# Performance work log

Hardware: AMD Instinct MI355X
Metric: run time of the kernel (lower is better)

The kernel has to match this reference:

```python
import jax, jax.numpy as jnp
import numpy as np

B, L, D, H, F = 2, 1024, 1024, 16, 4096
DH = D // H
EPS = 1e-6


def _layernorm(x, g, b, eps=1e-5):
    m = jnp.mean(x, axis=-1, keepdims=True)
    v = jnp.mean((x - m) ** 2, axis=-1, keepdims=True)
    return (x - m) / jnp.sqrt(v + eps) * g + b


def setup_inputs() -> dict:
    key = jax.random.key(0)
    ks = jax.random.split(key, 12)

    def w(k, shape):
        return jax.random.normal(k, shape, dtype=jnp.float32) * 0.02

    return {
        "inputs": jax.random.normal(ks[0], (B, L, D), dtype=jnp.float32),
        "attn_mask": jnp.zeros((L, L), dtype=jnp.bool_),
        "Wq": w(ks[1], (D, D)), "bq": jnp.zeros((D,), jnp.float32),
        "Wk": w(ks[2], (D, D)), "bk": jnp.zeros((D,), jnp.float32),
        "Wv": w(ks[3], (D, D)), "bv": jnp.zeros((D,), jnp.float32),
        "Wo": w(ks[4], (D, D)), "bo": jnp.zeros((D,), jnp.float32),
        "ln1_g": jnp.ones((D,), jnp.float32), "ln1_b": jnp.zeros((D,), jnp.float32),
        "W1": w(ks[5], (D, F)), "b1": jnp.zeros((F,), jnp.float32),
        "W2": w(ks[6], (F, D)), "b2": jnp.zeros((D,), jnp.float32),
        "ln2_g": jnp.ones((D,), jnp.float32), "ln2_b": jnp.zeros((D,), jnp.float32),
    }


def _decoder_layer(inputs, Wq, bq, Wk, bk, Wv, bv, Wo, bo,
                   ln1_g, ln1_b, W1, b1, W2, b2, ln2_g, ln2_b):
    Bn, Ln, Dn = inputs.shape

    def heads(W, b):
        # [B,L,D] -> [B,H,L,Dh]
        return (inputs @ W + b).reshape(Bn, Ln, H, DH).transpose(0, 2, 1, 3)

    q = jax.nn.sigmoid(heads(Wq, bq))  # kernel feature map
    k = jax.nn.sigmoid(heads(Wk, bk))
    v = heads(Wv, bv)

    normal = (jnp.arange(Ln, dtype=jnp.float32) + 1.0)[None, None, :]  # [1,1,L]

    sink_in = normal / jnp.einsum('bhld,bhld->bhl', q + EPS, jnp.cumsum(k, axis=2) + EPS)
    src_out = normal / jnp.einsum('bhld,bhld->bhl', k + EPS, jnp.cumsum(q, axis=2) + EPS)

    cons_sink = jnp.einsum('bhld,bhld->bhl', q + EPS,
                           jnp.cumsum(k * src_out[..., None], axis=2) + EPS) / normal
    cons_src = jnp.einsum('bhld,bhld->bhl', k + EPS,
                          jnp.cumsum(q * sink_in[..., None], axis=2) + EPS) / normal
    cons_src = jnp.clip(cons_src, -1.0, 1.0)

    sink_alloc = jax.nn.sigmoid(cons_sink)
    cons_src = jnp.exp(cons_src)
    src_comp = cons_src / jnp.cumsum(cons_src, axis=-1) * normal

    # causal linear attention: cumsum of outer products k v^T, contracted with q
    qs = q * (sink_in / normal)[..., None]           # [B,H,L,Dh]
    vs = v * src_comp[..., None]                     # [B,H,L,Dh]
    kv = jnp.cumsum(jnp.einsum('bhld,bhlm->bhldm', k, vs), axis=2)  # [B,H,L,Dh,Dh]
    x = jnp.einsum('bhld,bhldm->bhlm', qs, kv) * sink_alloc[..., None]

    x = x.transpose(0, 2, 1, 3).reshape(Bn, Ln, Dn)
    attn = x @ Wo + bo

    h = _layernorm(inputs + attn, ln1_g, ln1_b)
    ffn = jax.nn.gelu(h @ W1 + b1, approximate=False) @ W2 + b2
    return _layernorm(h + ffn, ln2_g, ln2_b)


def reference(inputs, attn_mask, Wq, bq, Wk, bk, Wv, bv, Wo, bo,
              ln1_g, ln1_b, W1, b1, W2, b2, ln2_g, ln2_b):
    # attn_mask is unused by the original module (causality comes from cumsum)
    return _decoder_layer(inputs, Wq, bq, Wk, bk, Wv, bv, Wo, bo,
                          ln1_g, ln1_b, W1, b1, W2, b2, ln2_g, ln2_b)
```

## Files before the change

### kernel.cpp

```cpp
#include <hip/hip_runtime.h>
#include <hip/hip_bf16.h>

#define EPS 1e-6f
#define NBH 32
#define LSEQ 1024
#define DHD 64

typedef unsigned short u16;
typedef __bf16 bf16x8 __attribute__((ext_vector_type(8)));
typedef float f32x4 __attribute__((ext_vector_type(4)));

__device__ inline u16 f2bf(float f){
  union { float f; unsigned u; } un; un.f = f;
  unsigned u = un.u;
  u += 0x7fffu + ((u >> 16) & 1u);
  return (u16)(u >> 16);
}

__device__ inline float wred64(float v){
#pragma unroll
  for (int off = 32; off > 0; off >>= 1) v += __shfl_xor(v, off, 64);
  return v;
}

__device__ inline float wscan64(float v, int lane){
  float run = v;
#pragma unroll
  for (int off = 1; off < 64; off <<= 1){
    float t = __shfl_up(run, off, 64);
    if (lane >= off) run += t;
  }
  return run;
}

__device__ inline float fast_sigmoid(float x){
  return 1.f / (1.f + __expf(-x));
}

__device__ inline void gload_lds16(const u16* g, u16* l){
  __builtin_amdgcn_global_load_lds(
      (const __attribute__((address_space(1))) unsigned int*)g,
      (__attribute__((address_space(3))) unsigned int*)l, 16, 0, 0);
}

__global__ __launch_bounds__(256) void f2bf_kernel(const float* __restrict__ in,
                                                   u16* __restrict__ out, int n4){
  int i = blockIdx.x * 256 + threadIdx.x;
  if (i < n4){
    float4 v = reinterpret_cast<const float4*>(in)[i];
    ushort4 o; o.x = f2bf(v.x); o.y = f2bf(v.y); o.z = f2bf(v.z); o.w = f2bf(v.w);
    reinterpret_cast<ushort4*>(out)[i] = o;
  }
}

__device__ inline void tr_tile2(const float* in, u16* out, int R, int C, int r0, int c0){
  __shared__ float tile[32][33];
  int x = threadIdx.x & 31, y = threadIdx.x >> 5;
#pragma unroll
  for (int j = 0; j < 4; j++)
    tile[y + j*8][x] = in[(size_t)(r0 + y + j*8) * C + c0 + x];
  __syncthreads();
#pragma unroll
  for (int j = 0; j < 4; j++)
    out[(size_t)(c0 + y + j*8) * R + r0 + x] = f2bf(tile[x][y + j*8]);
}

__global__ __launch_bounds__(256) void transpose4_f2bf(
    const float* __restrict__ w0, const float* __restrict__ w1,
    const float* __restrict__ w2, const float* __restrict__ w3,
    u16* __restrict__ dqkv, u16* __restrict__ dwo){
  int z = blockIdx.z;
  const float* in = (z == 0) ? w0 : (z == 1) ? w1 : (z == 2) ? w2 : w3;
  u16* out = (z < 3) ? (dqkv + (size_t)z * 1024 * 1024) : dwo;
  tr_tile2(in, out, 1024, 1024, blockIdx.y * 32, blockIdx.x * 32);
}

__global__ __launch_bounds__(256) void transpose2_f2bf(
    const float* __restrict__ w1, const float* __restrict__ w2,
    u16* __restrict__ d1, u16* __restrict__ d2){
  if (blockIdx.z == 0)
    tr_tile2(w1, d1, 1024, 4096, blockIdx.y * 32, blockIdx.x * 32);
  else
    tr_tile2(w2, d2, 4096, 1024, blockIdx.x * 32, blockIdx.y * 32);
}

__global__ __launch_bounds__(256) void bias_gather(const float* __restrict__ bq,
                                                   const float* __restrict__ bk,
                                                   const float* __restrict__ bv,
                                                   float* __restrict__ dst){
  int i = blockIdx.x * 256 + threadIdx.x;
  if (i < 3072){
    float v = (i < 1024) ? bq[i] : (i < 2048) ? bk[i - 1024] : bv[i - 2048];
    dst[i] = v;
  }
}

template<int BM, int BN, int ACT, int OM>
__global__ __launch_bounds__(256) void gemm_mfma(
    const u16* __restrict__ A, const u16* __restrict__ Bt,
    const float* __restrict__ bias, const float* __restrict__ resid,
    float* __restrict__ outF, u16* __restrict__ outB,
    int M, int N, int K)
{
  constexpr int BK = 64;
  constexpr int MI = BM / 32;
  constexpr int NJ = BN / 32;
  constexpr int RA = BM / 32;
  constexpr int RB = BN / 32;
  constexpr int NS = RA + RB;
  __shared__ u16 As[2][BM * BK];
  __shared__ u16 Bs[2][BN * BK];
  const int tid = threadIdx.x;
  const int lane = tid & 63, wave = tid >> 6;
  const int lrow = lane & 15, lg = lane >> 4;
  const int m0 = blockIdx.x * BM, n0 = blockIdx.y * BN;
  const int wm = (wave >> 1) * (BM / 2), wn = (wave & 1) * (BN / 2);

  const int ksz = K / gridDim.z;
  const int k_begin = blockIdx.z * ksz;
  const int k_end = k_begin + ksz;

  f32x4 acc[MI][NJ];
#pragma unroll
  for (int i = 0; i < MI; i++)
#pragma unroll
    for (int j = 0; j < NJ; j++) acc[i][j] = (f32x4){0.f, 0.f, 0.f, 0.f};

  const u16* Ab = A + (size_t)m0 * K;
  const u16* Bb = Bt + (size_t)n0 * K;

  const int s0 = ((0 * 4 + lg) ^ (lrow & 7)) * 8;
  const int s1 = ((1 * 4 + lg) ^ (lrow & 7)) * 8;

  auto STAGE = [&](int buf, int k0){
#pragma unroll
    for (int r = 0; r < RA; ++r){
      int c = r * 256 + tid;
      int row = c >> 3;
      int kk = ((c ^ row) & 7) << 3;
      gload_lds16(Ab + (size_t)row * K + k0 + kk, &As[buf][(r * 256 + wave * 64) * 8]);
    }
#pragma unroll
    for (int r = 0; r < RB; ++r){
      int c = r * 256 + tid;
      int row = c >> 3;
      int kk = ((c ^ row) & 7) << 3;
      gload_lds16(Bb + (size_t)row * K + k0 + kk, &Bs[buf][(r * 256 + wave * 64) * 8]);
    }
  };

  STAGE(0, k_begin);
  int cur = 0;
  for (int k0 = k_begin; k0 < k_end; k0 += BK){
    if (k0 + BK < k_end){
      STAGE(cur ^ 1, k0 + BK);
      if constexpr (NS == 8)      asm volatile("s_waitcnt vmcnt(8)" ::: "memory");
      else if constexpr (NS == 6) asm volatile("s_waitcnt vmcnt(6)" ::: "memory");
      else                        asm volatile("s_waitcnt vmcnt(0)" ::: "memory");
    } else {
      asm volatile("s_waitcnt vmcnt(0)" ::: "memory");
    }
    __builtin_amdgcn_s_barrier();
    __builtin_amdgcn_sched_barrier(0);
#pragma unroll
    for (int kh = 0; kh < 2; ++kh){
      const int ss = (kh == 0) ? s0 : s1;
      bf16x8 af[MI], bfv[NJ];
#pragma unroll
      for (int i = 0; i < MI; ++i)
        af[i] = *reinterpret_cast<const bf16x8*>(&As[cur][(wm + i * 16 + lrow) * BK + ss]);
#pragma unroll
      for (int j = 0; j < NJ; ++j)
        bfv[j] = *reinterpret_cast<const bf16x8*>(&Bs[cur][(wn + j * 16 + lrow) * BK + ss]);
#pragma unroll
      for (int i = 0; i < MI; ++i)
#pragma unroll
        for (int j = 0; j < NJ; ++j)
          acc[i][j] = __builtin_amdgcn_mfma_f32_16x16x32_bf16(af[i], bfv[j], acc[i][j], 0, 0, 0);
    }
    __builtin_amdgcn_s_barrier();
    cur ^= 1;
  }

#pragma unroll
  for (int i = 0; i < MI; ++i){
#pragma unroll
    for (int j = 0; j < NJ; ++j){
      int col = n0 + wn + j * 16 + lrow;
      float bv = (OM != 4 && bias) ? bias[col] : 0.f;
#pragma unroll
      for (int r = 0; r < 4; ++r){
        int row = m0 + wm + i * 16 + lg * 4 + r;
        float x = acc[i][j][r] + bv;
        if (OM == 1){
          if (col < 2048) x = fast_sigmoid(x);
          int which = col >> 10, cc = col & 1023, h = cc >> 6, d = cc & 63;
          int b = row >> 10, l = row & 1023;
          outF[(size_t)which * (2048ull * 1024) +
               (((size_t)(b * 16 + h)) * 1024 + l) * 64 + d] = x;
        } else if (OM == 4){
          outF[((size_t)blockIdx.z * M + row) * N + col] = x;
        } else {
          if (ACT == 2){
            float u = 0.7978845608f * (x + 0.044715f * x * x * x);
            float e = __expf(2.f * u);
            x = 0.5f * x * (2.f - 2.f / (e + 1.f));
          }
          outB[(size_t)row * N + col] = f2bf(x);
        }
      }
    }
  }
}

__global__ __launch_bounds__(256) void chunk_sums(const float* __restrict__ k, const float* __restrict__ q,
                                                  float* __restrict__ ck, float* __restrict__ cq){
  int blk = blockIdx.x;
  int lane = threadIdx.x & 63, wave = threadIdx.x >> 6;
  size_t base = (size_t)blk * 64 * DHD;
  float sk = 0.f, sq = 0.f;
  for (int l = wave * 16; l < wave * 16 + 16; l++){
    sk += k[base + l * 64 + lane];
    sq += q[base + l * 64 + lane];
  }
  __shared__ float rd[2][4][64];
  rd[0][wave][lane] = sk; rd[1][wave][lane] = sq;
  __syncthreads();
  if (wave == 0){
    ck[(size_t)blk * 64 + lane] = rd[0][0][lane] + rd[0][1][lane] + rd[0][2][lane] + rd[0][3][lane];
    cq[(size_t)blk * 64 + lane] = rd[1][0][lane] + rd[1][1][lane] + rd[1][2][lane] + rd[1][3][lane];
  }
}

__global__ __launch_bounds__(256) void sink_tile(
    const float* __restrict__ q, const float* __restrict__ k,
    const float* __restrict__ ck, const float* __restrict__ cq,
    float* __restrict__ sink_in, float* __restrict__ src_out,
    float* __restrict__ cso, float* __restrict__ cqsi)
{
  int blk = blockIdx.x, bh = blk >> 4, c = blk & 15;
  int tid = threadIdx.x, lane = tid & 63, wave = tid >> 6;
  __shared__ float qT[64][65], kT[64][65], G[64][66];
  __shared__ float PK[64], PQ[64];
  __shared__ float rk[64], rq[64], crk[64], crq[64], siv[64], sov[64];
  __shared__ float rd[2][4][64];
  size_t base = ((size_t)bh * LSEQ + c * 64) * DHD;
  const float* qb = q + base; const float* kb = k + base;
  for (int c4 = tid; c4 < 1024; c4 += 256){
    int l = c4 >> 4, d0 = (c4 & 15) * 4;
    float4 qv = *reinterpret_cast<const float4*>(qb + c4 * 4);
    qT[d0+0][l] = qv.x; qT[d0+1][l] = qv.y; qT[d0+2][l] = qv.z; qT[d0+3][l] = qv.w;
    float4 kv = *reinterpret_cast<const float4*>(kb + c4 * 4);
    kT[d0+0][l] = kv.x; kT[d0+1][l] = kv.y; kT[d0+2][l] = kv.z; kT[d0+3][l] = kv.w;
  }
  if (tid < 64){
    float pk = 0.f, pq = 0.f;
    for (int cc = 0; cc < c; cc++){
      pk += ck[((size_t)bh * 16 + cc) * 64 + tid];
      pq += cq[((size_t)bh * 16 + cc) * 64 + tid];
    }
    PK[tid] = pk; PQ[tid] = pq;
  }
  __syncthreads();
  float sumPK = wred64(PK[lane]);
  float sumPQ = wred64(PQ[lane]);
  {
    int l = lane, g = wave;
    float qrow[64];
#pragma unroll
    for (int d = 0; d < 64; d++) qrow[d] = qT[d][l];
    float p[16] = {};
    for (int d = 0; d < 64; d++){
      float qv = qrow[d];
#pragma unroll
      for (int j4 = 0; j4 < 4; j4++){
        float4 kk = *reinterpret_cast<const float4*>(&kT[d][g * 16 + j4 * 4]);
        p[j4*4+0] += qv * kk.x; p[j4*4+1] += qv * kk.y;
        p[j4*4+2] += qv * kk.z; p[j4*4+3] += qv * kk.w;
      }
    }
#pragma unroll
    for (int jj = 0; jj < 16; jj++) G[l][g * 16 + jj] = p[jj];
  }
  {
    float pk_ = 0.f, pq_ = 0.f;
#pragma unroll
    for (int d = wave * 16; d < wave * 16 + 16; d++){
      pk_ += kT[d][lane]; pq_ += qT[d][lane];
    }
    rd[0][wave][lane] = pk_; rd[1][wave][lane] = pq_;
  }
  __syncthreads();
  if (tid < 64){
    rk[tid] = rd[0][0][tid] + rd[0][1][tid] + rd[0][2][tid] + rd[0][3][tid];
    rq[tid] = rd[1][0][tid] + rd[1][1][tid] + rd[1][2][tid] + rd[1][3][tid];
  }
  __syncthreads();
  if (wave == 0)      crk[lane] = wscan64(rk[lane], lane);
  else if (wave == 1) crq[lane] = wscan64(rq[lane], lane);
  __syncthreads();
  {
    int l = lane;
    float p1 = 0.f, p2 = 0.f;
#pragma unroll
    for (int j = wave * 16; j < wave * 16 + 16; j++){
      float g1 = (j <= l) ? G[l][j] : 0.f;
      p1 += g1 + qT[j][l] * PK[j];
      float g2 = (j <= l) ? G[j][l] : 0.f;
      p2 += g2 + kT[j][l] * PQ[j];
    }
    rd[0][wave][l] = p1; rd[1][wave][l] = p2;
  }
  __syncthreads();
  const float EPS2 = 64.f * EPS * EPS;
  if (tid < 64){
    int l = tid;
    float s1 = rd[0][0][l] + rd[0][1][l] + rd[0][2][l] + rd[0][3][l];
    float s2 = rd[1][0][l] + rd[1][1][l] + rd[1][2][l] + rd[1][3][l];
    int L = c * 64 + l; float nrm = (float)(L + 1);
    float den1 = s1 + EPS * rq[l] + EPS * (sumPK + crk[l]) + EPS2;
    float den2 = s2 + EPS * rk[l] + EPS * (sumPQ + crq[l]) + EPS2;
    float si_ = nrm / den1, so_ = nrm / den2;
    sink_in[(size_t)bh * LSEQ + L] = si_;
    src_out[(size_t)bh * LSEQ + L] = so_;
    siv[l] = si_; sov[l] = so_;
  }
  __syncthreads();
  float s1 = 0.f, s2 = 0.f;
  for (int l = wave * 16; l < wave * 16 + 16; l++){
    s1 += sov[l] * kT[lane][l];
    s2 += siv[l] * qT[lane][l];
  }
  rd[0][wave][lane] = s1; rd[1][wave][lane] = s2;
  __syncthreads();
  if (wave == 0){
    cso [(size_t)blk * 64 + lane] = rd[0][0][lane] + rd[0][1][lane] + rd[0][2][lane] + rd[0][3][lane];
    cqsi[(size_t)blk * 64 + lane] = rd[1][0][lane] + rd[1][1][lane] + rd[1][2][lane] + rd[1][3][lane];
  }
}

__global__ __launch_bounds__(256) void cons_tile(
    const float* __restrict__ q, const float* __restrict__ k,
    const float* __restrict__ cso, const float* __restrict__ cqsi,
    const float* __restrict__ sink_in, const float* __restrict__ src_out,
    float* __restrict__ sa, float* __restrict__ ebuf)
{
  int blk = blockIdx.x, bh = blk >> 4, c = blk & 15;
  int tid = threadIdx.x, lane = tid & 63, wave = tid >> 6;
  __shared__ float qT[64][65], kT[64][65], G[64][66];
  __shared__ float PKso[64], PQsi[64];
  __shared__ float rk[64], rq[64], cwrk[64], cwrq[64], siv[64], sov[64];
  __shared__ float rd[2][4][64];
  size_t base = ((size_t)bh * LSEQ + c * 64) * DHD;
  const float* qb = q + base; const float* kb = k + base;
  for (int c4 = tid; c4 < 1024; c4 += 256){
    int l = c4 >> 4, d0 = (c4 & 15) * 4;
    float4 qv = *reinterpret_cast<const float4*>(qb + c4 * 4);
    qT[d0+0][l] = qv.x; qT[d0+1][l] = qv.y; qT[d0+2][l] = qv.z; qT[d0+3][l] = qv.w;
    float4 kv = *reinterpret_cast<const float4*>(kb + c4 * 4);
    kT[d0+0][l] = kv.x; kT[d0+1][l] = kv.y; kT[d0+2][l] = kv.z; kT[d0+3][l] = kv.w;
  }
  if (tid < 64){
    float pk = 0.f, pq = 0.f;
    for (int cc = 0; cc < c; cc++){
      pk += cso [((size_t)bh * 16 + cc) * 64 + tid];
      pq += cqsi[((size_t)bh * 16 + cc) * 64 + tid];
    }
    PKso[tid] = pk; PQsi[tid] = pq;
  } else if (tid < 128){
    int l = tid - 64;
    sov[l] = src_out[(size_t)bh * LSEQ + c * 64 + l];
    siv[l] = sink_in[(size_t)bh * LSEQ + c * 64 + l];
  }
  __syncthreads();
  float sumPKso = wred64(PKso[lane]);
  float sumPQsi = wred64(PQsi[lane]);
  {
    int l = lane, g = wave;
    float qrow[64];
#pragma unroll
    for (int d = 0; d < 64; d++) qrow[d] = qT[d][l];
    float p[16] = {};
    for (int d = 0; d < 64; d++){
      float qv = qrow[d];
#pragma unroll
      for (int j4 = 0; j4 < 4; j4++){
        float4 kk = *reinterpret_cast<const float4*>(&kT[d][g * 16 + j4 * 4]);
        p[j4*4+0] += qv * kk.x; p[j4*4+1] += qv * kk.y;
        p[j4*4+2] += qv * kk.z; p[j4*4+3] += qv * kk.w;
      }
    }
#pragma unroll
    for (int jj = 0; jj < 16; jj++) G[l][g * 16 + jj] = p[jj];
  }
  {
    float pk_ = 0.f, pq_ = 0.f;
#pragma unroll
    for (int d = wave * 16; d < wave * 16 + 16; d++){
      pk_ += kT[d][lane]; pq_ += qT[d][lane];
    }
    rd[0][wave][lane] = pk_; rd[1][wave][lane] = pq_;
  }
  __syncthreads();
  if (tid < 64){
    rk[tid] = rd[0][0][tid] + rd[0][1][tid] + rd[0][2][tid] + rd[0][3][tid];
    rq[tid] = rd[1][0][tid] + rd[1][1][tid] + rd[1][2][tid] + rd[1][3][tid];
  }
  __syncthreads();
  if (wave == 0)      cwrk[lane] = wscan64(sov[lane] * rk[lane], lane);
  else if (wave == 1) cwrq[lane] = wscan64(siv[lane] * rq[lane], lane);
  __syncthreads();
  {
    int l = lane;
    float p3 = 0.f, p4 = 0.f;
#pragma unroll
    for (int j = wave * 16; j < wave * 16 + 16; j++){
      float g3 = (j <= l) ? sov[j] * G[l][j] : 0.f;
      p3 += g3 + qT[j][l] * PKso[j];
      float g4 = (j <= l) ? siv[j] * G[j][l] : 0.f;
      p4 += g4 + kT[j][l] * PQsi[j];
    }
    rd[0][wave][l] = p3; rd[1][wave][l] = p4;
  }
  __syncthreads();
  const float EPS2 = 64.f * EPS * EPS;
  if (tid < 64){
    int l = tid;
    float s3 = rd[0][0][l] + rd[0][1][l] + rd[0][2][l] + rd[0][3][l];
    float s4 = rd[1][0][l] + rd[1][1][l] + rd[1][2][l] + rd[1][3][l];
    int L = c * 64 + l; float nrm = (float)(L + 1);
    float cs = (s3 + EPS * rq[l] + EPS * (sumPKso + cwrk[l]) + EPS2) / nrm;
    sa[(size_t)bh * LSEQ + L] = fast_sigmoid(cs);
    float c2 = (s4 + EPS * rk[l] + EPS * (sumPQsi + cwrq[l]) + EPS2) / nrm;
    c2 = fminf(1.f, fmaxf(-1.f, c2));
    ebuf[(size_t)bh * LSEQ + L] = __expf(c2);
  }
}

__global__ __launch_bounds__(64) void srccomp_kernel(const float* __restrict__ ebuf, float* __restrict__ sc){
  int bh = blockIdx.x; int lane = threadIdx.x;
  const float* eb = ebuf + (size_t)bh * LSEQ;
  float loc[16]; float s = 0.f;
#pragma unroll
  for (int i = 0; i < 16; i++){ loc[i] = eb[lane * 16 + i]; s += loc[i]; }
  float run = wscan64(s, lane);
  float acc = run - s;
  float* scb = sc + (size_t)bh * LSEQ;
#pragma unroll
  for (int i = 0; i < 16; i++){
    acc += loc[i];
    scb[lane * 16 + i] = loc[i] / acc * (float)(lane * 16 + i + 1);
  }
}

__global__ __launch_bounds__(256) void phaseA(const float* __restrict__ k, const float* __restrict__ v,
                                              const float* __restrict__ sc, float* __restrict__ S){
  int blk = blockIdx.x; int bh = blk >> 4, c = blk & 15;
  __shared__ float ks[64][68], vss[64][68];
  __shared__ float vc[64];
  int tid = threadIdx.x;
  size_t base = ((size_t)bh * LSEQ + c * 64) * DHD;
  const float* kb = k + base; const float* vb = v + base;
  if (tid < 64) vc[tid] = sc[(size_t)bh * LSEQ + c * 64 + tid];
  __syncthreads();
  for (int c4 = tid; c4 < 1024; c4 += 256){
    int l = c4 >> 4, d0 = (c4 & 15) * 4;
    *reinterpret_cast<float4*>(&ks[l][d0]) = *reinterpret_cast<const float4*>(kb + c4 * 4);
    float4 vv = *reinterpret_cast<const float4*>(vb + c4 * 4);
    float w = vc[l];
    vss[l][d0+0] = vv.x * w; vss[l][d0+1] = vv.y * w;
    vss[l][d0+2] = vv.z * w; vss[l][d0+3] = vv.w * w;
  }
  __syncthreads();
  int m = tid >> 2, dg = tid & 3;
  float acc[16] = {};
  for (int l = 0; l < 64; l++){
    float vm = vss[l][m];
#pragma unroll
    for (int d4 = 0; d4 < 4; d4++){
      float4 kk = *reinterpret_cast<const float4*>(&ks[l][dg * 16 + d4 * 4]);
      acc[d4*4+0] += vm * kk.x; acc[d4*4+1] += vm * kk.y;
      acc[d4*4+2] += vm * kk.z; acc[d4*4+3] += vm * kk.w;
    }
  }
  float* Sb = S + (size_t)blk * 4096 + m * 64 + dg * 16;
#pragma unroll
  for (int d4 = 0; d4 < 4; d4++)
    *reinterpret_cast<float4*>(Sb + d4 * 4) =
        make_float4(acc[d4*4], acc[d4*4+1], acc[d4*4+2], acc[d4*4+3]);
}

__global__ __launch_bounds__(256) void phaseB(const float* __restrict__ S, float* __restrict__ KVp){
  int blk = blockIdx.x; int bh = blk >> 4, c = blk & 15;
  int off = threadIdx.x * 16;
  float acc[16] = {};
  for (int cc = 0; cc < c; cc++){
    size_t idx = ((size_t)bh * 16 + cc) * 4096 + off;
#pragma unroll
    for (int t = 0; t < 4; t++){
      float4 sv = *reinterpret_cast<const float4*>(S + idx + t * 4);
      acc[t*4] += sv.x; acc[t*4+1] += sv.y; acc[t*4+2] += sv.z; acc[t*4+3] += sv.w;
    }
  }
  size_t oidx = ((size_t)bh * 16 + c) * 4096 + off;
#pragma unroll
  for (int t = 0; t < 4; t++)
    *reinterpret_cast<float4*>(KVp + oidx + t * 4) =
        make_float4(acc[t*4], acc[t*4+1], acc[t*4+2], acc[t*4+3]);
}

__global__ __launch_bounds__(256) void phaseC(const float* __restrict__ q, const float* __restrict__ k,
                                              const float* __restrict__ v, const float* __restrict__ KVp,
                                              const float* __restrict__ sink_in, const float* __restrict__ sc,
                                              const float* __restrict__ sa, u16* __restrict__ x){
  int blk = blockIdx.x; int bh = blk >> 4, c = blk & 15;
  int b = bh >> 4, h = bh & 15;
  __shared__ float qsT[64][65];
  __shared__ float kT[64][68];
  __shared__ float vss[64][68];
  __shared__ float kvs[64][68];
  __shared__ float Ps[64][66];
  __shared__ float qc[64], vc[64];
  int tid = threadIdx.x;
  size_t base = ((size_t)bh * LSEQ + c * 64) * DHD;
  const float* qb = q + base; const float* kb = k + base; const float* vb = v + base;
  const float* kvb = KVp + (size_t)blk * 4096;
  if (tid < 64){
    int L = c * 64 + tid;
    qc[tid] = sink_in[(size_t)bh * LSEQ + L] / (float)(L + 1);
    vc[tid] = sc[(size_t)bh * LSEQ + L];
  }
  __syncthreads();
  for (int c4 = tid; c4 < 1024; c4 += 256){
    int l = c4 >> 4, d0 = (c4 & 15) * 4;
    float qw = qc[l], vw = vc[l];
    float4 qv = *reinterpret_cast<const float4*>(qb + c4 * 4);
    qsT[d0+0][l] = qv.x * qw; qsT[d0+1][l] = qv.y * qw;
    qsT[d0+2][l] = qv.z * qw; qsT[d0+3][l] = qv.w * qw;
    float4 kv4 = *reinterpret_cast<const float4*>(kb + c4 * 4);
    kT[d0+0][l] = kv4.x; kT[d0+1][l] = kv4.y; kT[d0+2][l] = kv4.z; kT[d0+3][l] = kv4.w;
    float4 vv = *reinterpret_cast<const float4*>(vb + c4 * 4);
    vss[l][d0+0] = vv.x * vw; vss[l][d0+1] = vv.y * vw;
    vss[l][d0+2] = vv.z * vw; vss[l][d0+3] = vv.w * vw;
    *reinterpret_cast<float4*>(&kvs[l][d0]) = *reinterpret_cast<const float4*>(kvb + c4 * 4);
  }
  __syncthreads();
  int l = tid & 63, g = tid >> 6;
  float qrow[64];
#pragma unroll
  for (int d = 0; d < 64; d++) qrow[d] = qsT[d][l];

  float p[16] = {};
  for (int d = 0; d < 64; d++){
    float qv = qrow[d];
#pragma unroll
    for (int j4 = 0; j4 < 4; j4++){
      float4 kk = *reinterpret_cast<const float4*>(&kT[d][g * 16 + j4 * 4]);
      p[j4*4+0] += qv * kk.x; p[j4*4+1] += qv * kk.y;
      p[j4*4+2] += qv * kk.z; p[j4*4+3] += qv * kk.w;
    }
  }
#pragma unroll
  for (int jj = 0; jj < 16; jj++){
    int j = g * 16 + jj;
    Ps[l][j] = (j <= l) ? p[jj] : 0.f;
  }
  __syncthreads();

  float acc[16];
#pragma unroll
  for (int mm = 0; mm < 16; mm++){
    float a = 0.f;
#pragma unroll
    for (int d4 = 0; d4 < 16; d4++){
      float4 kv4 = *reinterpret_cast<const float4*>(&kvs[g * 16 + mm][d4 * 4]);
      a += qrow[d4*4+0]*kv4.x + qrow[d4*4+1]*kv4.y + qrow[d4*4+2]*kv4.z + qrow[d4*4+3]*kv4.w;
    }
    acc[mm] = a;
  }
  for (int j = 0; j < 64; j++){
    float pv = Ps[l][j];
#pragma unroll
    for (int m4 = 0; m4 < 4; m4++){
      float4 vv = *reinterpret_cast<const float4*>(&vss[j][g * 16 + m4 * 4]);
      acc[m4*4+0] += pv * vv.x; acc[m4*4+1] += pv * vv.y;
      acc[m4*4+2] += pv * vv.z; acc[m4*4+3] += pv * vv.w;
    }
  }
  float sav = sa[(size_t)bh * LSEQ + c * 64 + l];
  u16* xo = x + ((size_t)(b * 1024 + c * 64 + l)) * 1024 + h * 64 + g * 16;
#pragma unroll
  for (int mm = 0; mm < 16; mm++) xo[mm] = f2bf(acc[mm] * sav);
}

__global__ __launch_bounds__(256) void ln_fused2b(
    const float* __restrict__ p0, const float* __restrict__ p1,
    const float* __restrict__ resid, const float* __restrict__ bias,
    const float* __restrict__ g, const float* __restrict__ b,
    float* __restrict__ out, u16* __restrict__ outbf){
  int row = blockIdx.x; int tid = threadIdx.x;
  int lane = tid & 63, wave = tid >> 6;
  size_t off = (size_t)row * 1024 + tid * 4;
  float4 a0 = *reinterpret_cast<const float4*>(p0 + off);
  float4 a1 = *reinterpret_cast<const float4*>(p1 + off);
  float4 rr = *reinterpret_cast<const float4*>(resid + off);
  float4 bb = *reinterpret_cast<const float4*>(bias + tid * 4);
  float4 v = make_float4(a0.x + a1.x + rr.x + bb.x, a0.y + a1.y + rr.y + bb.y,
                         a0.z + a1.z + rr.z + bb.z, a0.w + a1.w + rr.w + bb.w);
  float s = v.x + v.y + v.z + v.w;
  float s2 = v.x*v.x + v.y*v.y + v.z*v.z + v.w*v.w;
  s = wred64(s); s2 = wred64(s2);
  __shared__ float red[2][4];
  if (lane == 0){ red[0][wave] = s; red[1][wave] = s2; }
  __syncthreads();
  float S = red[0][0] + red[0][1] + red[0][2] + red[0][3];
  float S2 = red[1][0] + red[1][1] + red[1][2] + red[1][3];
  float mean = S * (1.f / 1024.f);
  float var = S2 * (1.f / 1024.f) - mean * mean;
  float inv = rsqrtf(var + 1e-5f);
  float4 gv = *reinterpret_cast<const float4*>(g + tid * 4);
  float4 bv = *reinterpret_cast<const float4*>(b + tid * 4);
  float y0 = (v.x - mean) * inv * gv.x + bv.x;
  float y1 = (v.y - mean) * inv * gv.y + bv.y;
  float y2 = (v.z - mean) * inv * gv.z + bv.z;
  float y3 = (v.w - mean) * inv * gv.w + bv.w;
  *reinterpret_cast<float4*>(out + off) = make_float4(y0, y1, y2, y3);
  ushort4 o; o.x = f2bf(y0); o.y = f2bf(y1); o.z = f2bf(y2); o.w = f2bf(y3);
  *reinterpret_cast<ushort4*>(outbf + off) = o;
}

__global__ __launch_bounds__(256) void ln_fused4(
    const float* __restrict__ p0, const float* __restrict__ p1,
    const float* __restrict__ p2, const float* __restrict__ p3,
    const float* __restrict__ resid, const float* __restrict__ bias,
    const float* __restrict__ g, const float* __restrict__ b,
    float* __restrict__ out){
  int row = blockIdx.x; int tid = threadIdx.x;
  int lane = tid & 63, wave = tid >> 6;
  size_t off = (size_t)row * 1024 + tid * 4;
  float4 a0 = *reinterpret_cast<const float4*>(p0 + off);
  float4 a1 = *reinterpret_cast<const float4*>(p1 + off);
  float4 a2 = *reinterpret_cast<const float4*>(p2 + off);
  float4 a3 = *reinterpret_cast<const float4*>(p3 + off);
  float4 rr = *reinterpret_cast<const float4*>(resid + off);
  float4 bb = *reinterpret_cast<const float4*>(bias + tid * 4);
  float4 v = make_float4(a0.x + a1.x + a2.x + a3.x + rr.x + bb.x,
                         a0.y + a1.y + a2.y + a3.y + rr.y + bb.y,
                         a0.z + a1.z + a2.z + a3.z + rr.z + bb.z,
                         a0.w + a1.w + a2.w + a3.w + rr.w + bb.w);
  float s = v.x + v.y + v.z + v.w;
  float s2 = v.x*v.x + v.y*v.y + v.z*v.z + v.w*v.w;
  s = wred64(s); s2 = wred64(s2);
  __shared__ float red[2][4];
  if (lane == 0){ red[0][wave] = s; red[1][wave] = s2; }
  __syncthreads();
  float S = red[0][0] + red[0][1] + red[0][2] + red[0][3];
  float S2 = red[1][0] + red[1][1] + red[1][2] + red[1][3];
  float mean = S * (1.f / 1024.f);
  float var = S2 * (1.f / 1024.f) - mean * mean;
  float inv = rsqrtf(var + 1e-5f);
  float4 gv = *reinterpret_cast<const float4*>(g + tid * 4);
  float4 bv = *reinterpret_cast<const float4*>(b + tid * 4);
  float y0 = (v.x - mean) * inv * gv.x + bv.x;
  float y1 = (v.y - mean) * inv * gv.y + bv.y;
  float y2 = (v.z - mean) * inv * gv.z + bv.z;
  float y3 = (v.w - mean) * inv * gv.w + bv.w;
  *reinterpret_cast<float4*>(out + off) = make_float4(y0, y1, y2, y3);
}

extern "C" void kernel_launch(void* const* d_in, const int* in_sizes, int n_in,
                              void* d_out, int out_size, void* d_ws, size_t ws_size,
                              hipStream_t stream){
  (void)in_sizes; (void)n_in; (void)out_size; (void)ws_size;
  const float* inputs = (const float*)d_in[0];
  const float* Wq = (const float*)d_in[2];  const float* bq = (const float*)d_in[3];
  const float* Wk = (const float*)d_in[4];  const float* bk = (const float*)d_in[5];
  const float* Wv = (const float*)d_in[6];  const float* bv = (const float*)d_in[7];
  const float* Wo = (const float*)d_in[8];  const float* bo = (const float*)d_in[9];
  const float* ln1g = (const float*)d_in[10]; const float* ln1b = (const float*)d_in[11];
  const float* W1 = (const float*)d_in[12]; const float* b1 = (const float*)d_in[13];
  const float* W2 = (const float*)d_in[14]; const float* b2 = (const float*)d_in[15];
  const float* ln2g = (const float*)d_in[16]; const float* ln2b = (const float*)d_in[17];
  float* out = (float*)d_out;

  char* wsp = (char*)d_ws; size_t off = 0;
  auto alloc = [&](size_t bytes) -> void* {
    off = (off + 255) & ~(size_t)255;
    void* p = wsp + off; off += bytes; return p;
  };
  const size_t MD = (size_t)2048 * 1024;
  u16* Xbf    = (u16*)alloc(MD * 2);
  u16* WqkvT  = (u16*)alloc((size_t)3 * 1024 * 1024 * 2);
  u16* WoT    = (u16*)alloc((size_t)1024 * 1024 * 2);
  u16* W1T    = (u16*)alloc((size_t)4096 * 1024 * 2);
  u16* W2T    = (u16*)alloc((size_t)4096 * 1024 * 2);
  float* bqkv = (float*)alloc(3072 * 4);
  float* qkvb = (float*)alloc(3 * MD * 4);
  float* qb = qkvb; float* kb = qkvb + MD; float* vb = qkvb + 2 * MD;
  float* quad = (float*)alloc(4 * MD * 4);
  float* Sbuf = quad;
  float* KVp  = quad + MD;
  float* ckb  = (float*)alloc((size_t)512 * 64 * 4);
  float* cqb  = (float*)alloc((size_t)512 * 64 * 4);
  float* csob = (float*)alloc((size_t)512 * 64 * 4);
  float* cqsib= (float*)alloc((size_t)512 * 64 * 4);
  float* sink_in = (float*)alloc(NBH * LSEQ * 4);
  float* src_out = (float*)alloc(NBH * LSEQ * 4);
  float* sabuf   = (float*)alloc(NBH * LSEQ * 4);
  float* ebuf    = (float*)alloc(NBH * LSEQ * 4);
  float* scbuf   = (float*)alloc(NBH * LSEQ * 4);
  u16* xatt   = (u16*)alloc(MD * 2);
  u16* g1     = (u16*)alloc((size_t)2048 * 4096 * 2);
  float* part = quad;
  float* hbuf = vb;
  u16* hbf = (u16*)qb;

  f2bf_kernel<<<2048, 256, 0, stream>>>(inputs, Xbf, (int)(MD / 4));
  transpose4_f2bf<<<dim3(32, 32, 4), 256, 0, stream>>>(Wq, Wk, Wv, Wo, WqkvT, WoT);
  transpose2_f2bf<<<dim3(128, 32, 2), 256, 0, stream>>>(W1, W2, W1T, W2T);
  bias_gather<<<12, 256, 0, stream>>>(bq, bk, bv, bqkv);

  gemm_mfma<128, 64, 0, 1><<<dim3(16, 48), 256, 0, stream>>>(
      Xbf, WqkvT, bqkv, nullptr, qkvb, nullptr, 2048, 3072, 1024);

  chunk_sums<<<512, 256, 0, stream>>>(kb, qb, ckb, cqb);
  sink_tile<<<512, 256, 0, stream>>>(qb, kb, ckb, cqb, sink_in, src_out, csob, cqsib);
  cons_tile<<<512, 256, 0, stream>>>(qb, kb, csob, cqsib, sink_in, src_out, sabuf, ebuf);
  srccomp_kernel<<<32, 64, 0, stream>>>(ebuf, scbuf);

  phaseA<<<512, 256, 0, stream>>>(kb, vb, scbuf, Sbuf);
  phaseB<<<512, 256, 0, stream>>>(Sbuf, KVp);
  phaseC<<<512, 256, 0, stream>>>(qb, kb, vb, KVp, sink_in, scbuf, sabuf, xatt);

  gemm_mfma<128, 64, 0, 4><<<dim3(16, 16, 2), 256, 0, stream>>>(
      xatt, WoT, nullptr, nullptr, part, nullptr, 2048, 1024, 1024);
  ln_fused2b<<<2048, 256, 0, stream>>>(part, part + MD, inputs, bo, ln1g, ln1b, hbuf, hbf);

  gemm_mfma<128, 128, 2, 3><<<dim3(16, 32), 256, 0, stream>>>(
      hbf, W1T, b1, nullptr, nullptr, g1, 2048, 4096, 1024);
  gemm_mfma<128, 128, 0, 4><<<dim3(16, 8, 4), 256, 0, stream>>>(
      g1, W2T, nullptr, nullptr, part, nullptr, 2048, 1024, 4096);
  ln_fused4<<<2048, 256, 0, stream>>>(part, part + MD, part + 2 * MD, part + 3 * MD,
                                      hbuf, b2, ln2g, ln2b, out);
}
```

Baseline: 216.3 us.

## Merge prep kernels into one launch and fold prefix-sum phase into phaseC

The four preprocessing kernels (input bf16 cast, weight transposes, bias gather) are combined into a single kernel that dispatches on block index. The phaseB exclusive prefix sum over chunk KV states is removed, and each phaseC block now accumulates the preceding chunks' S matrices directly into shared memory. This also moves the Wo partial output buffer so it no longer overlaps Sbuf. The goal is to cut launch overhead and the KVp round trip through global memory. The cost is redundant reads of S across phaseC blocks, with later chunks reading up to 15 prior chunk states, plus scattered LDS stores.

```diff
diff --git a/kernel.cpp b/kernel.cpp
--- a/kernel.cpp
+++ b/kernel.cpp
@@ -43,16 +43,6 @@
       (__attribute__((address_space(3))) unsigned int*)l, 16, 0, 0);
 }
 
-__global__ __launch_bounds__(256) void f2bf_kernel(const float* __restrict__ in,
-                                                   u16* __restrict__ out, int n4){
-  int i = blockIdx.x * 256 + threadIdx.x;
-  if (i < n4){
-    float4 v = reinterpret_cast<const float4*>(in)[i];
-    ushort4 o; o.x = f2bf(v.x); o.y = f2bf(v.y); o.z = f2bf(v.z); o.w = f2bf(v.w);
-    reinterpret_cast<ushort4*>(out)[i] = o;
-  }
-}
-
 __device__ inline void tr_tile2(const float* in, u16* out, int R, int C, int r0, int c0){
   __shared__ float tile[32][33];
   int x = threadIdx.x & 31, y = threadIdx.x >> 5;
@@ -65,33 +55,41 @@
     out[(size_t)(c0 + y + j*8) * R + r0 + x] = f2bf(tile[x][y + j*8]);
 }
 
-__global__ __launch_bounds__(256) void transpose4_f2bf(
-    const float* __restrict__ w0, const float* __restrict__ w1,
-    const float* __restrict__ w2, const float* __restrict__ w3,
-    u16* __restrict__ dqkv, u16* __restrict__ dwo){
-  int z = blockIdx.z;
-  const float* in = (z == 0) ? w0 : (z == 1) ? w1 : (z == 2) ? w2 : w3;
-  u16* out = (z < 3) ? (dqkv + (size_t)z * 1024 * 1024) : dwo;
-  tr_tile2(in, out, 1024, 1024, blockIdx.y * 32, blockIdx.x * 32);
-}
-
-__global__ __launch_bounds__(256) void transpose2_f2bf(
-    const float* __restrict__ w1, const float* __restrict__ w2,
-    u16* __restrict__ d1, u16* __restrict__ d2){
-  if (blockIdx.z == 0)
-    tr_tile2(w1, d1, 1024, 4096, blockIdx.y * 32, blockIdx.x * 32);
-  else
-    tr_tile2(w2, d2, 4096, 1024, blockIdx.x * 32, blockIdx.y * 32);
-}
-
-__global__ __launch_bounds__(256) void bias_gather(const float* __restrict__ bq,
-                                                   const float* __restrict__ bk,
-                                                   const float* __restrict__ bv,
-                                                   float* __restrict__ dst){
-  int i = blockIdx.x * 256 + threadIdx.x;
-  if (i < 3072){
-    float v = (i < 1024) ? bq[i] : (i < 2048) ? bk[i - 1024] : bv[i - 2048];
-    dst[i] = v;
+__global__ __launch_bounds__(256) void prep_all(
+    const float* __restrict__ inputs, u16* __restrict__ Xbf,
+    const float* __restrict__ Wq, const float* __restrict__ Wk,
+    const float* __restrict__ Wv, const float* __restrict__ Wo,
+    u16* __restrict__ dqkv, u16* __restrict__ dwo,
+    const float* __restrict__ W1, const float* __restrict__ W2,
+    u16* __restrict__ d1, u16* __restrict__ d2,
+    const float* __restrict__ bq, const float* __restrict__ bk,
+    const float* __restrict__ bv, float* __restrict__ bqkv)
+{
+  int b = blockIdx.x;
+  if (b < 2048){
+    int i = b * 256 + threadIdx.x;
+    float4 v = reinterpret_cast<const float4*>(inputs)[i];
+    ushort4 o; o.x = f2bf(v.x); o.y = f2bf(v.y); o.z = f2bf(v.z); o.w = f2bf(v.w);
+    reinterpret_cast<ushort4*>(Xbf)[i] = o;
+  } else if (b < 6144){
+    int t = b - 2048;
+    int z = t >> 10, rem = t & 1023;
+    int bx = rem & 31, by = rem >> 5;
+    const float* in = (z == 0) ? Wq : (z == 1) ? Wk : (z == 2) ? Wv : Wo;
+    u16* out = (z < 3) ? (dqkv + (size_t)z * 1024 * 1024) : dwo;
+    tr_tile2(in, out, 1024, 1024, by * 32, bx * 32);
+  } else if (b < 14336){
+    int t = b - 6144;
+    int z = t >> 12, rem = t & 4095;
+    int bx = rem & 127, by = rem >> 7;
+    if (z == 0) tr_tile2(W1, d1, 1024, 4096, by * 32, bx * 32);
+    else        tr_tile2(W2, d2, 4096, 1024, bx * 32, by * 32);
+  } else {
+    int i = (b - 14336) * 256 + threadIdx.x;
+    if (i < 3072){
+      float v = (i < 1024) ? bq[i] : (i < 2048) ? bk[i - 1024] : bv[i - 2048];
+      bqkv[i] = v;
+    }
   }
 }
 
@@ -490,27 +488,8 @@
         make_float4(acc[d4*4], acc[d4*4+1], acc[d4*4+2], acc[d4*4+3]);
 }
 
-__global__ __launch_bounds__(256) void phaseB(const float* __restrict__ S, float* __restrict__ KVp){
-  int blk = blockIdx.x; int bh = blk >> 4, c = blk & 15;
-  int off = threadIdx.x * 16;
-  float acc[16] = {};
-  for (int cc = 0; cc < c; cc++){
-    size_t idx = ((size_t)bh * 16 + cc) * 4096 + off;
-#pragma unroll
-    for (int t = 0; t < 4; t++){
-      float4 sv = *reinterpret_cast<const float4*>(S + idx + t * 4);
-      acc[t*4] += sv.x; acc[t*4+1] += sv.y; acc[t*4+2] += sv.z; acc[t*4+3] += sv.w;
-    }
-  }
-  size_t oidx = ((size_t)bh * 16 + c) * 4096 + off;
-#pragma unroll
-  for (int t = 0; t < 4; t++)
-    *reinterpret_cast<float4*>(KVp + oidx + t * 4) =
-        make_float4(acc[t*4], acc[t*4+1], acc[t*4+2], acc[t*4+3]);
-}
-
 __global__ __launch_bounds__(256) void phaseC(const float* __restrict__ q, const float* __restrict__ k,
-                                              const float* __restrict__ v, const float* __restrict__ KVp,
+                                              const float* __restrict__ v, const float* __restrict__ S,
                                               const float* __restrict__ sink_in, const float* __restrict__ sc,
                                               const float* __restrict__ sa, u16* __restrict__ x){
   int blk = blockIdx.x; int bh = blk >> 4, c = blk & 15;
@@ -524,11 +503,28 @@
   int tid = threadIdx.x;
   size_t base = ((size_t)bh * LSEQ + c * 64) * DHD;
   const float* qb = q + base; const float* kb = k + base; const float* vb = v + base;
-  const float* kvb = KVp + (size_t)blk * 4096;
   if (tid < 64){
     int L = c * 64 + tid;
     qc[tid] = sink_in[(size_t)bh * LSEQ + L] / (float)(L + 1);
     vc[tid] = sc[(size_t)bh * LSEQ + L];
+  }
+  {
+    int off16 = tid * 16;
+    float accp[16] = {};
+    for (int cc = 0; cc < c; cc++){
+      size_t idx = ((size_t)bh * 16 + cc) * 4096 + off16;
+#pragma unroll
+      for (int t4 = 0; t4 < 4; t4++){
+        float4 sv = *reinterpret_cast<const float4*>(S + idx + t4 * 4);
+        accp[t4*4+0] += sv.x; accp[t4*4+1] += sv.y;
+        accp[t4*4+2] += sv.z; accp[t4*4+3] += sv.w;
+      }
+    }
+#pragma unroll
+    for (int e = 0; e < 16; e++){
+      int j = off16 + e;
+      kvs[j >> 6][j & 63] = accp[e];
+    }
   }
   __syncthreads();
   for (int c4 = tid; c4 < 1024; c4 += 256){
@@ -542,7 +538,6 @@
     float4 vv = *reinterpret_cast<const float4*>(vb + c4 * 4);
     vss[l][d0+0] = vv.x * vw; vss[l][d0+1] = vv.y * vw;
     vss[l][d0+2] = vv.z * vw; vss[l][d0+3] = vv.w * vw;
-    *reinterpret_cast<float4*>(&kvs[l][d0]) = *reinterpret_cast<const float4*>(kvb + c4 * 4);
   }
   __syncthreads();
   int l = tid & 63, g = tid >> 6;
@@ -699,7 +694,6 @@
   float* qb = qkvb; float* kb = qkvb + MD; float* vb = qkvb + 2 * MD;
   float* quad = (float*)alloc(4 * MD * 4);
   float* Sbuf = quad;
-  float* KVp  = quad + MD;
   float* ckb  = (float*)alloc((size_t)512 * 64 * 4);
   float* cqb  = (float*)alloc((size_t)512 * 64 * 4);
   float* csob = (float*)alloc((size_t)512 * 64 * 4);
@@ -715,10 +709,8 @@
   float* hbuf = vb;
   u16* hbf = (u16*)qb;
 
-  f2bf_kernel<<<2048, 256, 0, stream>>>(inputs, Xbf, (int)(MD / 4));
-  transpose4_f2bf<<<dim3(32, 32, 4), 256, 0, stream>>>(Wq, Wk, Wv, Wo, WqkvT, WoT);
-  transpose2_f2bf<<<dim3(128, 32, 2), 256, 0, stream>>>(W1, W2, W1T, W2T);
-  bias_gather<<<12, 256, 0, stream>>>(bq, bk, bv, bqkv);
+  prep_all<<<14348, 256, 0, stream>>>(inputs, Xbf, Wq, Wk, Wv, Wo, WqkvT, WoT,
+                                      W1, W2, W1T, W2T, bq, bk, bv, bqkv);
 
   gemm_mfma<128, 64, 0, 1><<<dim3(16, 48), 256, 0, stream>>>(
       Xbf, WqkvT, bqkv, nullptr, qkvb, nullptr, 2048, 3072, 1024);
@@ -729,12 +721,12 @@
   srccomp_kernel<<<32, 64, 0, stream>>>(ebuf, scbuf);
 
   phaseA<<<512, 256, 0, stream>>>(kb, vb, scbuf, Sbuf);
-  phaseB<<<512, 256, 0, stream>>>(Sbuf, KVp);
-  phaseC<<<512, 256, 0, stream>>>(qb, kb, vb, KVp, sink_in, scbuf, sabuf, xatt);
-
+  phaseC<<<512, 256, 0, stream>>>(qb, kb, vb, Sbuf, sink_in, scbuf, sabuf, xatt);
+
+  float* wopart = quad + 2 * MD;
   gemm_mfma<128, 64, 0, 4><<<dim3(16, 16, 2), 256, 0, stream>>>(
-      xatt, WoT, nullptr, nullptr, part, nullptr, 2048, 1024, 1024);
-  ln_fused2b<<<2048, 256, 0, stream>>>(part, part + MD, inputs, bo, ln1g, ln1b, hbuf, hbf);
+      xatt, WoT, nullptr, nullptr, wopart, nullptr, 2048, 1024, 1024);
+  ln_fused2b<<<2048, 256, 0, stream>>>(wopart, wopart + MD, inputs, bo, ln1g, ln1b, hbuf, hbf);
 
   gemm_mfma<128, 128, 2, 3><<<dim3(16, 32), 256, 0, stream>>>(
       hbf, W1T, b1, nullptr, nullptr, g1, 2048, 4096, 1024);
```

Measured after the change: 206.9 us. 4.3% less time.
